# Performance work log

Hardware: AMD Instinct MI355X
Metric: run time of the kernel (lower is better)

The kernel has to match this reference:

```python
import jax, jax.numpy as jnp
import numpy as np

N, M, K, R, D = 2048, 64, 2, 512, 1024   # seq len, chunk size, neighbours, neighbour len, model dim
H, L = 16, 1024                           # heads, layer_size
LCH = N // M                              # number of chunks l = 32
DH = L // H
SCALE = 1.0 / (D ** 0.5)                  # source scales by input dim, not head dim


def setup_inputs() -> dict:
    key = jax.random.key(0)
    ks = jax.random.split(key, 6)
    s = 0.02
    return {
        "x": jax.random.normal(ks[0], (N, D), jnp.float32),
        "neighbours": jax.random.normal(ks[1], (LCH, K, R, D), jnp.float32),
        "Wq": jax.random.normal(ks[2], (L, D), jnp.float32) * s,
        "Wk": jax.random.normal(ks[3], (L, D), jnp.float32) * s,
        "Wv": jax.random.normal(ks[4], (L, D), jnp.float32) * s,
        "Wo": jax.random.normal(ks[5], (D, L), jnp.float32) * s,
    }


def _attend(q_in, ctx, Wq, Wk, Wv, Wo):
    # q_in: (B, Q, D) queries; ctx: (B, K, R, D) retrieved neighbours.
    # Batches the per-chunk, per-neighbour Attention calls of the source in one pass,
    # then means over the K neighbour axis (reduce 'k m d -> m d', 'mean').
    B, Q = q_in.shape[0], q_in.shape[1]
    q = (q_in @ Wq.T).reshape(B, Q, H, DH)                     # (B,Q,H,DH)
    kk = (ctx @ Wk.T).reshape(B, K, R, H, DH)                  # (B,K,R,H,DH)
    vv = (ctx @ Wv.T).reshape(B, K, R, H, DH)
    scores = jnp.einsum('bqhe,bkrhe->bkhrq', q, kk) * SCALE    # (B,K,H,R,Q)
    # FAITHFUL quirk: source softmaxes over the QUERY axis (last dim of 'b k q')
    w = jax.nn.softmax(scores, axis=-1)
    o = jnp.einsum('bkhrq,bkrhe->bkqhe', w, vv).reshape(B, K, Q, L)
    z = jnp.einsum('bkql,dl->bkqd', o, Wo)                     # output projection (dropout=0)
    return z.mean(axis=1)                                      # mean over neighbours -> (B,Q,D)


def reference(x, neighbours, Wq, Wk, Wv, Wo):
    # attending_chunks: shift input left by m-1, zero-pad bottom, chunk into (l, m, d)
    att = jnp.concatenate([x[M - 1:], jnp.zeros((M - 1, D), x.dtype)], axis=0).reshape(LCH, M, D)
    # main loop over chunks u in [0, l-2] and their k neighbours, fully batched
    main = _attend(att[:LCH - 1], neighbours[:LCH - 1], Wq, Wk, Wv, Wo)   # (l-1, M, D)
    # last token attends to neighbours[-1]
    last = _attend(x[-1][None, None, :], neighbours[-1][None], Wq, Wk, Wv, Wo)  # (1,1,D)
    body = jnp.concatenate([main.reshape(-1, D), att[-1]], axis=0)        # (N, D)
    # pad top with m-1 zeros, keep first n rows
    out = jnp.concatenate([jnp.zeros((M - 1, D), x.dtype), body[:N - M + 1]], axis=0)
    out = out.at[:M - 1].set(x[:M - 1])
    out = out.at[-1].set(last[0, 0])
    return out
```

## Files before the change

### kernel.cpp

```cpp
#include <hip/hip_runtime.h>
#include <hip/hip_bf16.h>


using u16 = unsigned short;
using u32 = unsigned int;

typedef float  f32x4   __attribute__((ext_vector_type(4)));
typedef __bf16 bf16x8v __attribute__((ext_vector_type(8)));
typedef __bf16 bf16x4v __attribute__((ext_vector_type(4)));
typedef short  s16x4   __attribute__((ext_vector_type(4)));
typedef u16    u16x8   __attribute__((ext_vector_type(8)));
typedef u16    u16x4v  __attribute__((ext_vector_type(4)));

#define SCALE_LOG2E (1.4426950408889634f / 32.0f)

__device__ __forceinline__ u16 f2b(float f){ return __builtin_bit_cast(u16, (__bf16)f); }
__device__ __forceinline__ int swz(int row, int cb){ return row*128 + (cb ^ ((row & 7) << 4)); }

__device__ __forceinline__ void gl_lds16(const void* g, void* l) {
    __builtin_amdgcn_global_load_lds(
        (const __attribute__((address_space(1))) unsigned int*)(unsigned long long)g,
        (__attribute__((address_space(3))) unsigned int*)(unsigned int)(unsigned long long)l,
        16, 0, 0);
}

template<int OM>
__global__ __launch_bounds__(512, 2)
void gemm256(const u16* __restrict__ Ap, int lda,
             const u16* __restrict__ Bp, int ldb,
             void* __restrict__ Cp, void* __restrict__ Cp2,
             int M, int Kc, int nNt)
{
    __shared__ char Ls[131072];
    char* const Abase = Ls;
    char* const Bbase = Ls + 65536;

    const int tid  = threadIdx.x;
    const int lane = tid & 63, wave = tid >> 6;
    const int li = lane & 15, lg = lane >> 4;
    const int wr = wave >> 2, wc = wave & 3;

    const int nwg  = gridDim.x;
    const int lin  = blockIdx.x;
    const int lin2 = (lin & 7) * (nwg >> 3) + (lin >> 3);
    const long bm = (long)(lin2 / nNt) * 256;
    const long bn = (long)(lin2 % nNt) * 256;

    const int srow = tid >> 3;
    const int scol = ((tid & 7) ^ (srow & 7)) << 3;

    auto stageA = [&](int t, int hh) {
        char* d = Abase + (t & 1)*32768 + hh*16384 + wave*1024;
        long r0 = bm + hh*128 + srow;      if (r0 >= M) r0 = M - 1;
        long r1 = bm + hh*128 + 64 + srow; if (r1 >= M) r1 = M - 1;
        gl_lds16(Ap + r0*(long)lda + (long)t*64 + scol, d);
        gl_lds16(Ap + r1*(long)lda + (long)t*64 + scol, d + 8192);
    };
    auto stageB = [&](int t, int hh) {
        char* d = Bbase + (t & 1)*32768 + hh*16384 + wave*1024;
        long r0 = bn + hh*128 + srow;
        gl_lds16(Bp + r0*(long)ldb + (long)t*64 + scol, d);
        gl_lds16(Bp + (r0 + 64)*(long)ldb + (long)t*64 + scol, d + 8192);
    };

    const int NT = Kc >> 6;

    stageB(0, 0); stageB(0, 1); stageA(0, 0);
    stageA(0, 1); stageB(1, 0);
    asm volatile("s_waitcnt vmcnt(4)" ::: "memory");
    asm volatile("s_barrier" ::: "memory");

    const int swx = (li & 7) << 4;
    const int cb0 = (lg*16) ^ swx;
    const int cb1 = (64 + lg*16) ^ swx;
    const int arb = li;
    const int brb = (wc & 1)*64 + li;

    f32x4 acc[8][4] = {};
    bf16x8v a[4], b[4];

#define MFMA16(MH)                                                              \
    __builtin_amdgcn_s_setprio(1);                                              \
    _Pragma("unroll") for (int mt = 0; mt < 4; mt++)                            \
        _Pragma("unroll") for (int nt = 0; nt < 4; nt++)                        \
            acc[(MH)*4 + mt][nt] = __builtin_amdgcn_mfma_f32_16x16x32_bf16(     \
                a[mt], b[nt], acc[(MH)*4 + mt][nt], 0, 0, 0);                   \
    __builtin_amdgcn_s_setprio(0);

#define BAR_IN()  asm volatile("s_barrier" ::: "memory");                       \
                  asm volatile("s_waitcnt lgkmcnt(0)" ::: "memory");            \
                  __builtin_amdgcn_sched_barrier(0);
#define BAR_OUT() asm volatile("s_barrier" ::: "memory");

    for (int t = 0; t < NT; ++t) {
        char* At = Abase + (t & 1)*32768 + wr*16384;
        char* Bt = Bbase + (t & 1)*32768 + (wc >> 1)*16384;

        #pragma unroll
        for (int mt = 0; mt < 4; mt++) a[mt] = *(const bf16x8v*)(At + (arb + mt*16)*128 + cb0);
        #pragma unroll
        for (int nt = 0; nt < 4; nt++) b[nt] = *(const bf16x8v*)(Bt + (brb + nt*16)*128 + cb0);
        if (t + 1 < NT) stageB(t + 1, 1);
        BAR_IN(); MFMA16(0);
        if (t + 1 < NT) { asm volatile("s_waitcnt vmcnt(4)" ::: "memory"); }
        else            { asm volatile("s_waitcnt vmcnt(0)" ::: "memory"); }
        BAR_OUT();
        #pragma unroll
        for (int mt = 0; mt < 4; mt++) a[mt] = *(const bf16x8v*)(At + (arb + 64 + mt*16)*128 + cb0);
        if (t + 1 < NT) stageA(t + 1, 0);
        BAR_IN(); MFMA16(1); BAR_OUT();
        #pragma unroll
        for (int mt = 0; mt < 4; mt++) a[mt] = *(const bf16x8v*)(At + (arb + mt*16)*128 + cb1);
        #pragma unroll
        for (int nt = 0; nt < 4; nt++) b[nt] = *(const bf16x8v*)(Bt + (brb + nt*16)*128 + cb1);
        if (t + 1 < NT) stageA(t + 1, 1);
        BAR_IN(); MFMA16(0); BAR_OUT();
        #pragma unroll
        for (int mt = 0; mt < 4; mt++) a[mt] = *(const bf16x8v*)(At + (arb + 64 + mt*16)*128 + cb1);
        if (t + 2 < NT) stageB(t + 2, 0);
        BAR_IN(); MFMA16(1);
        if      (t + 2 < NT) { asm volatile("s_waitcnt vmcnt(4)" ::: "memory"); }
        else if (t + 1 < NT) { asm volatile("s_waitcnt vmcnt(2)" ::: "memory"); }
        BAR_OUT();
    }
#undef MFMA16
#undef BAR_IN
#undef BAR_OUT

    if (OM == 3 && bn >= 1024) {
        u16* Vt = (u16*)Cp2;
        #pragma unroll
        for (int ai = 0; ai < 8; ai++) {
            const int m0 = wr*128 + (ai >> 2)*64 + (ai & 3)*16 + lg*4;
            #pragma unroll
            for (int nt = 0; nt < 4; nt++) {
                const int n = wc*64 + nt*16 + li;
                f32x4 c = acc[ai][nt];
                bf16x4v w;
                #pragma unroll
                for (int j = 0; j < 4; j++) w[j] = (__bf16)c[j];
                *(bf16x4v*)(Ls + n*512 + ((m0*2) ^ ((n & 31) << 4))) = w;
            }
        }
        __syncthreads();
        const int n    = tid >> 1;
        const int half = (tid & 1) * 128;
        u16* dst = Vt + (bn - 1024 + n)*32768L + bm + half;
        #pragma unroll
        for (int i = 0; i < 16; i++) {
            const int mb = (half + i*8) * 2;
            uint4 v = *(const uint4*)(Ls + n*512 + (mb ^ ((n & 31) << 4)));
            *(uint4*)(dst + i*8) = v;
        }
    } else if (OM == 3) {
        u16* Ka = (u16*)Cp;
        #pragma unroll
        for (int ai = 0; ai < 8; ai++) {
            #pragma unroll
            for (int nt = 0; nt < 4; nt++) {
                f32x4 c = acc[ai][nt];
                const long row0 = bm + wr*128 + (ai >> 2)*64 + (ai & 3)*16 + lg*4;
                const long col  = bn + wc*64 + nt*16 + li;
                #pragma unroll
                for (int j = 0; j < 4; j++) {
                    long rg = row0 + j;
                    if (rg < M) Ka[rg*1024 + col] = f2b(c[j]);
                }
            }
        }
    }
}

template<bool AF32, int OM>
__global__ __launch_bounds__(256)
void gemm128(const void* __restrict__ Ap, int lda,
             const u16* __restrict__ Bp, int ldb,
             void* __restrict__ Cp, void* __restrict__ Cp2,
             int M, int Kc, int row_off, int nNt)
{
    __shared__ char As[128*128];
    __shared__ char Bs[128*128];
    const int tid  = threadIdx.x;
    const int lane = tid & 63, wave = tid >> 6;
    const int li = lane & 15, lg = lane >> 4;
    const int wr = wave >> 1, wc = wave & 1;

    const int nwg  = gridDim.x;
    const int lin  = blockIdx.x;
    const int lin2 = (lin & 7) * (nwg >> 3) + (lin >> 3);
    const long bm = (long)(lin2 / nNt) * 128;
    const long bn = (long)(lin2 % nNt) * 128;

    const int grow = wave*32 + (lane >> 3);
    const int gcol = ((lane & 7) ^ (lane >> 3)) << 3;
    const int sr = tid >> 1, sc = (tid & 1) * 32;
    long arow_f = bm + sr; if (arow_f >= M) arow_f = M - 1;
    long arow_g[4];
    #pragma unroll
    for (int j = 0; j < 4; j++) {
        long r = bm + grow + j*8;
        arow_g[j] = (r < M) ? r : (M - 1);
    }

    f32x4 acc[4][4] = {};

    for (int k0 = 0; k0 < Kc; k0 += 64) {
        float4 a4[8];
        if (AF32) {
            const float4* ap = (const float4*)((const float*)Ap + arow_f*lda + k0 + sc);
            #pragma unroll
            for (int i = 0; i < 8; i++) a4[i] = ap[i];
        }
        __syncthreads();
        if (!AF32) {
            #pragma unroll
            for (int j = 0; j < 4; j++)
                gl_lds16((const u16*)Ap + arow_g[j]*(long)lda + k0 + gcol,
                         As + (wave*4 + j)*1024);
        }
        #pragma unroll
        for (int j = 0; j < 4; j++)
            gl_lds16(Bp + (bn + grow + j*8)*(long)ldb + k0 + gcol,
                     Bs + (wave*4 + j)*1024);
        if (AF32) {
            #pragma unroll
            for (int i = 0; i < 4; i++) {
                float4 f0 = a4[2*i], f1 = a4[2*i+1];
                bf16x8v w;
                w[0]=(__bf16)f0.x; w[1]=(__bf16)f0.y; w[2]=(__bf16)f0.z; w[3]=(__bf16)f0.w;
                w[4]=(__bf16)f1.x; w[5]=(__bf16)f1.y; w[6]=(__bf16)f1.z; w[7]=(__bf16)f1.w;
                *(bf16x8v*)(As + swz(sr, sc*2 + i*16)) = w;
            }
        }
        __syncthreads();
        #pragma unroll
        for (int es = 0; es < 2; es++) {
            bf16x8v af[4], bfv[4];
            #pragma unroll
            for (int mt = 0; mt < 4; mt++)
                af[mt] = *(const bf16x8v*)(As + swz(wr*64 + mt*16 + li, es*64 + lg*16));
            #pragma unroll
            for (int nt = 0; nt < 4; nt++)
                bfv[nt] = *(const bf16x8v*)(Bs + swz(wc*64 + nt*16 + li, es*64 + lg*16));
            #pragma unroll
            for (int mt = 0; mt < 4; mt++)
                #pragma unroll
                for (int nt = 0; nt < 4; nt++)
                    acc[mt][nt] = __builtin_amdgcn_mfma_f32_16x16x32_bf16(
                        af[mt], bfv[nt], acc[mt][nt], 0, 0, 0);
        }
    }

    #pragma unroll
    for (int mt = 0; mt < 4; mt++) {
        #pragma unroll
        for (int nt = 0; nt < 4; nt++) {
            f32x4 c = acc[mt][nt];
            const long row0 = bm + wr*64 + mt*16 + lg*4;
            const long col  = bn + wc*64 + nt*16 + li;
            if (OM == 0) {
                u16* C = (u16*)Cp;
                #pragma unroll
                for (int j = 0; j < 4; j++) {
                    long rg = row0 + j;
                    if (rg < M) C[rg*1024 + col] = f2b(c[j]);
                }
            } else if (OM == 2) {
                float* C = (float*)Cp;
                #pragma unroll
                for (int j = 0; j < 4; j++) {
                    long rg = row0 + j;
                    if (rg < M) C[(row_off + rg)*1024 + col] = c[j];
                }
            } else {
                if (col < 1024) {
                    u16* Ka = (u16*)Cp;
                    #pragma unroll
                    for (int j = 0; j < 4; j++) Ka[(row0 + j)*1024 + col] = f2b(c[j]);
                } else {
                    u16* Vt = (u16*)Cp2;
                    bf16x4v w;
                    #pragma unroll
                    for (int j = 0; j < 4; j++) w[j] = (__bf16)c[j];
                    *(bf16x4v*)(Vt + (col - 1024)*32768L + row0) = w;
                }
            }
        }
    }
}

__global__ __launch_bounds__(256)
void attn_kernel(const u16* __restrict__ Qa, const u16* __restrict__ Ka,
                 const u16* __restrict__ Vt, u16* __restrict__ Om)
{
    const int u = blockIdx.x, h = blockIdx.y;
    const int tid = threadIdx.x;
    const int lane = tid & 63, wave = tid >> 6;
    const int li = lane & 15, lg = lane >> 4;

    bf16x8v qf[4][2];
    #pragma unroll
    for (int qt = 0; qt < 4; qt++)
        #pragma unroll
        for (int es = 0; es < 2; es++)
            qf[qt][es] = *(const bf16x8v*)(Qa + (long)(63 + u*64 + qt*16 + li)*1024
                                              + h*64 + es*32 + lg*8);

    f32x4 acc[4][4] = {};

    for (int it = wave; it < 64; it += 4) {
        const int k = it >> 5, rsub = it & 31;
        const long kr = (long)u*1024 + k*512 + rsub*16;

        bf16x8v a0 = *(const bf16x8v*)(Ka + (kr + li)*1024 + h*64 + lg*8);
        bf16x8v a1 = *(const bf16x8v*)(Ka + (kr + li)*1024 + h*64 + 32 + lg*8);
        s16x4 va[4];
        #pragma unroll
        for (int et = 0; et < 4; et++)
            va[et] = *(const s16x4*)(Vt + (long)(h*64 + et*16 + li)*32768 + kr + lg*4);

        f32x4 s[4];
        #pragma unroll
        for (int qt = 0; qt < 4; qt++) {
            f32x4 c = {};
            c = __builtin_amdgcn_mfma_f32_16x16x32_bf16(a0, qf[qt][0], c, 0, 0, 0);
            c = __builtin_amdgcn_mfma_f32_16x16x32_bf16(a1, qf[qt][1], c, 0, 0, 0);
            s[qt] = c;
        }
        float p[4][4];
        #pragma unroll
        for (int qt = 0; qt < 4; qt++)
            #pragma unroll
            for (int j = 0; j < 4; j++)
                p[qt][j] = __builtin_amdgcn_exp2f(s[qt][j]);
        float rz[4];
        #pragma unroll
        for (int j = 0; j < 4; j++) {
            float z = p[0][j] + p[1][j] + p[2][j] + p[3][j];
            z += __shfl_xor(z, 1); z += __shfl_xor(z, 2);
            z += __shfl_xor(z, 4); z += __shfl_xor(z, 8);
            rz[j] = __builtin_amdgcn_rcpf(z);
        }
        s16x4 wf[4];
        #pragma unroll
        for (int qt = 0; qt < 4; qt++) {
            bf16x4v w;
            #pragma unroll
            for (int j = 0; j < 4; j++) w[j] = (__bf16)(p[qt][j] * rz[j]);
            wf[qt] = __builtin_bit_cast(s16x4, w);
        }
        #pragma unroll
        for (int et = 0; et < 4; et++)
            #pragma unroll
            for (int qt = 0; qt < 4; qt++)
                acc[et][qt] = __builtin_amdgcn_mfma_f32_16x16x16bf16_1k(
                    va[et], wf[qt], acc[et][qt], 0, 0, 0);
    }

    __shared__ float Osum[64*64];
    for (int w = 0; w < 4; w++) {
        if (wave == w) {
            #pragma unroll
            for (int et = 0; et < 4; et++)
                #pragma unroll
                for (int qt = 0; qt < 4; qt++)
                    #pragma unroll
                    for (int j = 0; j < 4; j++) {
                        int e = et*16 + lg*4 + j, q = qt*16 + li;
                        if (w == 0) Osum[e*64 + q]  = acc[et][qt][j];
                        else        Osum[e*64 + q] += acc[et][qt][j];
                    }
        }
        __syncthreads();
    }
    const int q = tid & 63, e0 = (tid >> 6) * 16;
    u16x8 o0, o1;
    #pragma unroll
    for (int i = 0; i < 8; i++) {
        o0[i] = f2b(0.5f * Osum[(e0 + i    )*64 + q]);
        o1[i] = f2b(0.5f * Osum[(e0 + 8 + i)*64 + q]);
    }
    u16* dst = Om + (long)(u*64 + q)*1024 + h*64 + e0;
    *(u16x8*)dst       = o0;
    *(u16x8*)(dst + 8) = o1;
}

__global__ __launch_bounds__(256)
void convert_w(const float* __restrict__ Wq, const float* __restrict__ Wk,
               const float* __restrict__ Wv, const float* __restrict__ Wo,
               u16* __restrict__ dst)
{
    int idx = blockIdx.x*256 + threadIdx.x;
    int w   = idx >> 18;
    int off = (idx & 262143) << 2;
    const float* src = (w == 0) ? Wq : (w == 1) ? Wk : (w == 2) ? Wv : Wo;
    float scv = (w == 0) ? SCALE_LOG2E : 1.0f;
    float4 v = *(const float4*)(src + off);
    u16x4v o = { f2b(v.x*scv), f2b(v.y*scv), f2b(v.z*scv), f2b(v.w*scv) };
    *(u16x4v*)(dst + (long)w*1048576 + off) = o;
}

__global__ __launch_bounds__(256)
void convert_a(const float* __restrict__ src, u16* __restrict__ dst, int n8)
{
    int i = blockIdx.x*256 + threadIdx.x;
    const int stride = gridDim.x*256;
    for (; i < n8; i += stride) {
        float4 f0 = ((const float4*)src)[2*i], f1 = ((const float4*)src)[2*i+1];
        u16x8 o = { f2b(f0.x), f2b(f0.y), f2b(f0.z), f2b(f0.w),
                    f2b(f1.x), f2b(f1.y), f2b(f1.z), f2b(f1.w) };
        ((u16x8*)dst)[i] = o;
    }
}

__global__ __launch_bounds__(256)
void last_kernel(const u16* __restrict__ Vt, u16* __restrict__ Om)
{
    const int row  = blockIdx.x*4 + (threadIdx.x >> 6);
    const int lane = threadIdx.x & 63;
    const u16* p = Vt + (long)row*32768 + 31*1024 + lane*16;
    float s = 0.f;
    #pragma unroll
    for (int hf = 0; hf < 2; hf++) {
        bf16x8v v = *(const bf16x8v*)(p + hf*8);
        #pragma unroll
        for (int i = 0; i < 8; i++) s += (float)v[i];
    }
    #pragma unroll
    for (int m = 1; m < 64; m <<= 1) s += __shfl_xor(s, m);
    if (lane == 0) Om[(long)1984*1024 + row] = f2b(0.5f * s);
}

__global__ __launch_bounds__(256)
void copy_head(const float* __restrict__ x, float* __restrict__ out)
{
    int i = blockIdx.x*256 + threadIdx.x;
    ((float4*)out)[i] = ((const float4*)x)[i];
}

extern "C" void kernel_launch(void* const* d_in, const int* in_sizes, int n_in,
                              void* d_out, int out_size, void* d_ws, size_t ws_size,
                              hipStream_t stream)
{
    const float* x  = (const float*)d_in[0];
    const float* nb = (const float*)d_in[1];
    const float* Wq = (const float*)d_in[2];
    const float* Wk = (const float*)d_in[3];
    const float* Wv = (const float*)d_in[4];
    const float* Wo = (const float*)d_in[5];
    float* out = (float*)d_out;
    char*  ws  = (char*)d_ws;

    if (ws_size < (size_t)144*1024*1024) return;
    const bool big = ws_size >= (size_t)212*1024*1024;
    u16* wW  = (u16*)ws;
    u16* Qa  = (u16*)(ws + (size_t) 8*1024*1024);
    u16* Om  = (u16*)(ws + (size_t)12*1024*1024);
    u16* Ka  = (u16*)(ws + (size_t)16*1024*1024);
    u16* Vt  = (u16*)(ws + (size_t)80*1024*1024);
    u16* Anb = (u16*)(ws + (size_t)144*1024*1024);
    u16* xb  = (u16*)(ws + (size_t)208*1024*1024);
    u16* wWq = wW, *wWk = wW + 1048576, *wWo = wW + 3*1048576;

    convert_w<<<dim3(4096), dim3(256), 0, stream>>>(Wq, Wk, Wv, Wo, wW);

    if (big) {
        convert_a<<<dim3(2048), dim3(256), 0, stream>>>(nb, Anb, 4194304);
        convert_a<<<dim3(512),  dim3(256), 0, stream>>>(x,  xb,  262144);
        gemm128<false, 0><<<dim3(128), dim3(256), 0, stream>>>(
            xb, 1024, wWq, 1024, Qa, nullptr, 2048, 1024, 0, 8);
        gemm256<3><<<dim3(1024), dim3(512), 0, stream>>>(
            Anb, 1024, wWk, 1024, Ka, Vt, 32768, 1024, 8);
    } else {
        gemm128<true, 0><<<dim3(128), dim3(256), 0, stream>>>(
            x, 1024, wWq, 1024, Qa, nullptr, 2048, 1024, 0, 8);
        gemm128<true, 3><<<dim3(4096), dim3(256), 0, stream>>>(
            nb, 1024, wWk, 1024, Ka, Vt, 32768, 1024, 0, 16);
    }

    attn_kernel<<<dim3(31, 16), dim3(256), 0, stream>>>(Qa, Ka, Vt, Om);
    last_kernel<<<dim3(256),    dim3(256), 0, stream>>>(Vt, Om);

    gemm128<false, 2><<<dim3(128), dim3(256), 0, stream>>>(
        Om, 1024, wWo, 1024, out, nullptr, 1985, 1024, 63, 8);
    copy_head<<<dim3(63), dim3(256), 0, stream>>>(x, out);
}
```

Measured before the change: 267.8 us.

## Restructure gemm256 main loop with double register buffers and fewer barriers; fuse conversions

The 256x256 GEMM main loop now keeps two A register buffers, so LDS reads for the next MFMA group overlap the current group. Per-iteration barriers drop from eight to two, and prefetch staging is reordered. Staging pointers are precomputed and the row clamps and bounds checks are removed, which relies on M being a multiple of 256. The three fp32-to-bf16 conversion launches are merged into one grid-stride kernel to cut launch overhead. The risks are extra register pressure and a possible LDS race from the reduced barriers and changed vmcnt waits.

```diff
diff --git a/kernel.cpp b/kernel.cpp
--- a/kernel.cpp
+++ b/kernel.cpp
@@ -49,83 +49,80 @@
     const int srow = tid >> 3;
     const int scol = ((tid & 7) ^ (srow & 7)) << 3;
 
-    auto stageA = [&](int t, int hh) {
+    const u16* const pA0 = Ap + (bm + srow)*(long)lda + scol;
+    const u16* const pA1 = Ap + (bm + 128 + srow)*(long)lda + scol;
+    const u16* const pB0 = Bp + (bn + srow)*(long)ldb + scol;
+    const u16* const pB1 = Bp + (bn + 128 + srow)*(long)ldb + scol;
+    const long l64a = 64*(long)lda, l64b = 64*(long)ldb;
+
+    auto stA = [&](int t, int hh) {
         char* d = Abase + (t & 1)*32768 + hh*16384 + wave*1024;
-        long r0 = bm + hh*128 + srow;      if (r0 >= M) r0 = M - 1;
-        long r1 = bm + hh*128 + 64 + srow; if (r1 >= M) r1 = M - 1;
-        gl_lds16(Ap + r0*(long)lda + (long)t*64 + scol, d);
-        gl_lds16(Ap + r1*(long)lda + (long)t*64 + scol, d + 8192);
+        const u16* p = (hh ? pA1 : pA0) + (long)t*64;
+        gl_lds16(p, d);
+        gl_lds16(p + l64a, d + 8192);
     };
-    auto stageB = [&](int t, int hh) {
+    auto stB = [&](int t, int hh) {
         char* d = Bbase + (t & 1)*32768 + hh*16384 + wave*1024;
-        long r0 = bn + hh*128 + srow;
-        gl_lds16(Bp + r0*(long)ldb + (long)t*64 + scol, d);
-        gl_lds16(Bp + (r0 + 64)*(long)ldb + (long)t*64 + scol, d + 8192);
+        const u16* p = (hh ? pB1 : pB0) + (long)t*64;
+        gl_lds16(p, d);
+        gl_lds16(p + l64b, d + 8192);
     };
 
     const int NT = Kc >> 6;
 
-    stageB(0, 0); stageB(0, 1); stageA(0, 0);
-    stageA(0, 1); stageB(1, 0);
-    asm volatile("s_waitcnt vmcnt(4)" ::: "memory");
+    stB(0, 0); stB(0, 1); stA(0, 0); stA(0, 1); stB(1, 0);
+    asm volatile("s_waitcnt vmcnt(2)" ::: "memory");
     asm volatile("s_barrier" ::: "memory");
 
     const int swx = (li & 7) << 4;
     const int cb0 = (lg*16) ^ swx;
     const int cb1 = (64 + lg*16) ^ swx;
-    const int arb = li;
     const int brb = (wc & 1)*64 + li;
 
     f32x4 acc[8][4] = {};
-    bf16x8v a[4], b[4];
-
-#define MFMA16(MH)                                                              \
+    bf16x8v av[4], aw[4], bv[4];
+
+#define MFMA16(MH, AA, BB)                                                      \
     __builtin_amdgcn_s_setprio(1);                                              \
     _Pragma("unroll") for (int mt = 0; mt < 4; mt++)                            \
         _Pragma("unroll") for (int nt = 0; nt < 4; nt++)                        \
             acc[(MH)*4 + mt][nt] = __builtin_amdgcn_mfma_f32_16x16x32_bf16(     \
-                a[mt], b[nt], acc[(MH)*4 + mt][nt], 0, 0, 0);                   \
+                (AA)[mt], (BB)[nt], acc[(MH)*4 + mt][nt], 0, 0, 0);             \
     __builtin_amdgcn_s_setprio(0);
-
-#define BAR_IN()  asm volatile("s_barrier" ::: "memory");                       \
-                  asm volatile("s_waitcnt lgkmcnt(0)" ::: "memory");            \
-                  __builtin_amdgcn_sched_barrier(0);
-#define BAR_OUT() asm volatile("s_barrier" ::: "memory");
+#define RDA(DST, OFS, CB)                                                       \
+    _Pragma("unroll") for (int i = 0; i < 4; i++)                               \
+        (DST)[i] = *(const bf16x8v*)(At + (li + (OFS) + i*16)*128 + (CB));
+#define RDB(DST, CB)                                                            \
+    _Pragma("unroll") for (int i = 0; i < 4; i++)                               \
+        (DST)[i] = *(const bf16x8v*)(Bt + (brb + i*16)*128 + (CB));
 
     for (int t = 0; t < NT; ++t) {
         char* At = Abase + (t & 1)*32768 + wr*16384;
         char* Bt = Bbase + (t & 1)*32768 + (wc >> 1)*16384;
-
-        #pragma unroll
-        for (int mt = 0; mt < 4; mt++) a[mt] = *(const bf16x8v*)(At + (arb + mt*16)*128 + cb0);
-        #pragma unroll
-        for (int nt = 0; nt < 4; nt++) b[nt] = *(const bf16x8v*)(Bt + (brb + nt*16)*128 + cb0);
-        if (t + 1 < NT) stageB(t + 1, 1);
-        BAR_IN(); MFMA16(0);
-        if (t + 1 < NT) { asm volatile("s_waitcnt vmcnt(4)" ::: "memory"); }
-        else            { asm volatile("s_waitcnt vmcnt(0)" ::: "memory"); }
-        BAR_OUT();
-        #pragma unroll
-        for (int mt = 0; mt < 4; mt++) a[mt] = *(const bf16x8v*)(At + (arb + 64 + mt*16)*128 + cb0);
-        if (t + 1 < NT) stageA(t + 1, 0);
-        BAR_IN(); MFMA16(1); BAR_OUT();
-        #pragma unroll
-        for (int mt = 0; mt < 4; mt++) a[mt] = *(const bf16x8v*)(At + (arb + mt*16)*128 + cb1);
-        #pragma unroll
-        for (int nt = 0; nt < 4; nt++) b[nt] = *(const bf16x8v*)(Bt + (brb + nt*16)*128 + cb1);
-        if (t + 1 < NT) stageA(t + 1, 1);
-        BAR_IN(); MFMA16(0); BAR_OUT();
-        #pragma unroll
-        for (int mt = 0; mt < 4; mt++) a[mt] = *(const bf16x8v*)(At + (arb + 64 + mt*16)*128 + cb1);
-        if (t + 2 < NT) stageB(t + 2, 0);
-        BAR_IN(); MFMA16(1);
-        if      (t + 2 < NT) { asm volatile("s_waitcnt vmcnt(4)" ::: "memory"); }
-        else if (t + 1 < NT) { asm volatile("s_waitcnt vmcnt(2)" ::: "memory"); }
-        BAR_OUT();
+        const bool s1 = (t + 1 < NT), s2 = (t + 2 < NT);
+
+        RDA(av, 0, cb0); RDB(bv, cb0);
+        if (s1) { stB(t + 1, 1); stA(t + 1, 0); }
+        RDA(aw, 64, cb0);
+        __builtin_amdgcn_sched_barrier(0);
+        MFMA16(0, av, bv);
+        if (s1) stA(t + 1, 1);
+        RDA(av, 0, cb1);
+        __builtin_amdgcn_sched_barrier(0);
+        MFMA16(1, aw, bv);
+        RDB(bv, cb1); RDA(aw, 64, cb1);
+        __builtin_amdgcn_sched_barrier(0);
+        MFMA16(0, av, bv);
+        asm volatile("s_barrier" ::: "memory");
+        if (s2) stB(t + 2, 0);
+        MFMA16(1, aw, bv);
+        if      (s2) { asm volatile("s_waitcnt vmcnt(2)" ::: "memory"); }
+        else if (s1) { asm volatile("s_waitcnt vmcnt(0)" ::: "memory"); }
+        asm volatile("s_barrier" ::: "memory");
     }
 #undef MFMA16
-#undef BAR_IN
-#undef BAR_OUT
+#undef RDA
+#undef RDB
 
     if (OM == 3 && bn >= 1024) {
         u16* Vt = (u16*)Cp2;
@@ -162,10 +159,8 @@
                 const long row0 = bm + wr*128 + (ai >> 2)*64 + (ai & 3)*16 + lg*4;
                 const long col  = bn + wc*64 + nt*16 + li;
                 #pragma unroll
-                for (int j = 0; j < 4; j++) {
-                    long rg = row0 + j;
-                    if (rg < M) Ka[rg*1024 + col] = f2b(c[j]);
-                }
+                for (int j = 0; j < 4; j++)
+                    Ka[(row0 + j)*1024 + col] = f2b(c[j]);
             }
         }
     }
@@ -386,30 +381,35 @@
 }
 
 __global__ __launch_bounds__(256)
-void convert_w(const float* __restrict__ Wq, const float* __restrict__ Wk,
-               const float* __restrict__ Wv, const float* __restrict__ Wo,
-               u16* __restrict__ dst)
-{
-    int idx = blockIdx.x*256 + threadIdx.x;
-    int w   = idx >> 18;
-    int off = (idx & 262143) << 2;
-    const float* src = (w == 0) ? Wq : (w == 1) ? Wk : (w == 2) ? Wv : Wo;
-    float scv = (w == 0) ? SCALE_LOG2E : 1.0f;
-    float4 v = *(const float4*)(src + off);
-    u16x4v o = { f2b(v.x*scv), f2b(v.y*scv), f2b(v.z*scv), f2b(v.w*scv) };
-    *(u16x4v*)(dst + (long)w*1048576 + off) = o;
-}
-
-__global__ __launch_bounds__(256)
-void convert_a(const float* __restrict__ src, u16* __restrict__ dst, int n8)
-{
-    int i = blockIdx.x*256 + threadIdx.x;
+void convert_all(const float* __restrict__ Wq, const float* __restrict__ Wk,
+                 const float* __restrict__ Wv, const float* __restrict__ Wo,
+                 const float* __restrict__ nb, const float* __restrict__ x,
+                 u16* __restrict__ wW, u16* __restrict__ Anb,
+                 u16* __restrict__ xb, int doA)
+{
+    const int NW = 524288, NN = 4194304, NX = 262144;
+    const int tot = doA ? (NW + NN + NX) : NW;
     const int stride = gridDim.x*256;
-    for (; i < n8; i += stride) {
-        float4 f0 = ((const float4*)src)[2*i], f1 = ((const float4*)src)[2*i+1];
-        u16x8 o = { f2b(f0.x), f2b(f0.y), f2b(f0.z), f2b(f0.w),
-                    f2b(f1.x), f2b(f1.y), f2b(f1.z), f2b(f1.w) };
-        ((u16x8*)dst)[i] = o;
+    for (int i = blockIdx.x*256 + threadIdx.x; i < tot; i += stride) {
+        const float* s; u16* d; float sc = 1.0f;
+        if (i < NW) {
+            int w = i >> 17;
+            long off = (long)(i & 131071) * 8;
+            s = (w == 0) ? Wq : (w == 1) ? Wk : (w == 2) ? Wv : Wo;
+            s += off;
+            d = wW + (long)w*1048576 + off;
+            if (w == 0) sc = SCALE_LOG2E;
+        } else if (i < NW + NN) {
+            long off = (long)(i - NW) * 8;
+            s = nb + off; d = Anb + off;
+        } else {
+            long off = (long)(i - NW - NN) * 8;
+            s = x + off; d = xb + off;
+        }
+        float4 f0 = ((const float4*)s)[0], f1 = ((const float4*)s)[1];
+        u16x8 o = { f2b(f0.x*sc), f2b(f0.y*sc), f2b(f0.z*sc), f2b(f0.w*sc),
+                    f2b(f1.x*sc), f2b(f1.y*sc), f2b(f1.z*sc), f2b(f1.w*sc) };
+        *(u16x8*)d = o;
     }
 }
 
@@ -462,11 +462,10 @@
     u16* xb  = (u16*)(ws + (size_t)208*1024*1024);
     u16* wWq = wW, *wWk = wW + 1048576, *wWo = wW + 3*1048576;
 
-    convert_w<<<dim3(4096), dim3(256), 0, stream>>>(Wq, Wk, Wv, Wo, wW);
+    convert_all<<<dim3(4096), dim3(256), 0, stream>>>(
+        Wq, Wk, Wv, Wo, nb, x, wW, Anb, xb, big ? 1 : 0);
 
     if (big) {
-        convert_a<<<dim3(2048), dim3(256), 0, stream>>>(nb, Anb, 4194304);
-        convert_a<<<dim3(512),  dim3(256), 0, stream>>>(x,  xb,  262144);
         gemm128<false, 0><<<dim3(128), dim3(256), 0, stream>>>(
             xb, 1024, wWq, 1024, Qa, nullptr, 2048, 1024, 0, 8);
         gemm256<3><<<dim3(1024), dim3(512), 0, stream>>>(
```

Measured after the change: 257.0 us. 1.04x faster.
